# Kernel optimization log

Hardware: AMD Instinct MI355X
Metric: run time of the kernel (lower is better)

The kernel has to match this reference:

```python
import jax, jax.numpy as jnp
import numpy as np


def setup_inputs() -> dict:
    key = jax.random.key(0)
    k1, k2 = jax.random.split(key)
    N, L, C = 64, 256, 384
    x = jax.random.normal(k1, (N, L, C), dtype=jnp.float32)
    # frame counts per phoneme, 1..16
    durations = jax.random.randint(k2, (N, L), 1, 17, dtype=jnp.int32)
    # expand_max_len = max over batch of total duration (static Python int)
    mel_max_length = int(jnp.max(jnp.sum(durations, axis=-1)))
    return {"x": x, "durations": durations, "mel_max_length": mel_max_length}


def reference(x, durations, mel_max_length):
    # Equivalent to: alignment[n, t, j] = 1 if starts[n,j] <= t < csum[n,j];
    # output = alignment @ x. Implemented as a direct gather via cumulative
    # durations (searchsorted), avoiding the O(N*T*L) one-hot matmul.
    N, L, C = x.shape
    csum = jnp.cumsum(durations, axis=-1)            # [N, L] exclusive end per phoneme
    t = jnp.arange(mel_max_length)                   # [T]
    # source phoneme index for each output frame: first j with t < csum[j]
    idx = jax.vmap(lambda c: jnp.searchsorted(c, t, side='right'))(csum)  # [N, T]
    total = csum[:, -1]                              # [N] total frames per example
    valid = t[None, :] < total[:, None]              # [N, T]
    idx = jnp.minimum(idx, L - 1)
    out = jnp.take_along_axis(x, idx[..., None], axis=1)   # [N, T, C]
    out = jnp.where(valid[..., None], out, jnp.zeros((), dtype=x.dtype))
    mel_pos = jnp.arange(1, mel_max_length + 1, dtype=jnp.int64)[None, :]  # [1, T]
    return out, mel_pos
```

## Files before the change

### kernel.cpp

```cpp
#include <hip/hip_runtime.h>

#define N_B    64
#define L_IN   256
#define C_DIM  384
#define C4     (C_DIM / 4)
#define F4_PER_BLOCK 2048
#define ITERS  (F4_PER_BLOCK / 256)
#define SPLIT  4

typedef float vfloat4 __attribute__((ext_vector_type(4)));

__global__ __launch_bounds__(256) void lr_idx_kernel(const int* __restrict__ dur,
                                                     int* __restrict__ idx_out,
                                                     float* __restrict__ melpos,
                                                     int melmax) {
    __shared__ int csum[L_IN];
    const int n    = blockIdx.x & 63;
    const int part = blockIdx.x >> 6;
    const int tid  = (int)threadIdx.x;

    csum[tid] = dur[n * L_IN + tid];
    __syncthreads();
    #pragma unroll
    for (int off = 1; off < L_IN; off <<= 1) {
        int add = (tid >= off) ? csum[tid - off] : 0;
        __syncthreads();
        csum[tid] += add;
        __syncthreads();
    }
    const int total = csum[L_IN - 1];

    const int per  = (melmax + SPLIT - 1) / SPLIT;
    const int tbeg = part * per;
    const int tend = min(tbeg + per, melmax);
    for (int t = tbeg + tid; t < tend; t += 256) {
        int r = -1;
        if (t < total) {
            int lo = 0, hi = L_IN;
            #pragma unroll
            for (int s = 0; s < 8; ++s) {
                int mid = (lo + hi) >> 1;
                if (csum[mid] <= t) lo = mid + 1; else hi = mid;
            }
            r = (lo < (L_IN - 1)) ? lo : (L_IN - 1);
        }
        idx_out[n * melmax + t] = r;
        if (n == 0) melpos[t] = (float)(t + 1);
    }
}

__global__ __launch_bounds__(256) void lr_gather_kernel(const vfloat4* __restrict__ x,
                                                        const int* __restrict__ idx,
                                                        vfloat4* __restrict__ out,
                                                        int melmax, int chunks_per_n) {
    __shared__ int r_tab[32];

    const int j      = (int)blockIdx.x;
    const int xcd    = j & 7;
    const int s      = j >> 3;
    const int n      = xcd + 8 * (s / chunks_per_n);
    const int bchunk = s % chunks_per_n;
    const int tid    = (int)threadIdx.x;

    const int row_f4 = melmax * C4;
    const int start  = bchunk * F4_PER_BLOCK;
    if (start >= row_f4) return;
    const bool full  = (start + F4_PER_BLOCK) <= row_f4;
    const int end    = full ? (start + F4_PER_BLOCK) : row_f4;

    const int t0   = start / C4;
    const int tcnt = (end - 1) / C4 - t0 + 1;
    if (tid < tcnt) r_tab[tid] = idx[n * melmax + t0 + tid];
    __syncthreads();

    const size_t obase = (size_t)n * row_f4;
    if (full) {
        vfloat4 v[ITERS];
        #pragma unroll
        for (int i = 0; i < ITERS; ++i) {
            const int off = start + tid + 256 * i;
            const int t   = off / C4;
            const int c4  = off - t * C4;
            const int r   = r_tab[t - t0];
            const int rc  = (r >= 0) ? r : 0;
            vfloat4 tmp = x[(n * L_IN + rc) * C4 + c4];
            v[i] = (r >= 0) ? tmp : (vfloat4)0.f;
        }
        #pragma unroll
        for (int i = 0; i < ITERS; ++i) {
            out[obase + start + tid + 256 * i] = v[i];
        }
    } else {
        for (int off = start + tid; off < end; off += 256) {
            const int t  = off / C4;
            const int c4 = off - t * C4;
            const int r  = r_tab[t - t0];
            vfloat4 v = (vfloat4)0.f;
            if (r >= 0) v = x[(n * L_IN + r) * C4 + c4];
            out[obase + off] = v;
        }
    }
}

extern "C" void kernel_launch(void* const* d_in, const int* in_sizes, int n_in,
                              void* d_out, int out_size, void* d_ws, size_t ws_size,
                              hipStream_t stream) {
    const float* x  = (const float*)d_in[0];
    const int* dur  = (const int*)d_in[1];
    const int melmax = out_size / (N_B * C_DIM + 1);

    int* idxbuf = (int*)d_ws;
    float* mp   = (float*)d_out + (size_t)N_B * melmax * C_DIM;

    lr_idx_kernel<<<N_B * SPLIT, 256, 0, stream>>>(dur, idxbuf, mp, melmax);

    const int row_f4 = melmax * C4;
    const int chunks_per_n = (row_f4 + F4_PER_BLOCK - 1) / F4_PER_BLOCK;
    lr_gather_kernel<<<chunks_per_n * N_B, 256, 0, stream>>>(
        (const vfloat4*)x, idxbuf, (vfloat4*)d_out, melmax, chunks_per_n);
}
```

Baseline: 252.3 us.

## Fuse duration scan and index search into the gather kernel

```diff
diff --git a/kernel.cpp b/kernel.cpp
--- a/kernel.cpp
+++ b/kernel.cpp
@@ -6,53 +6,15 @@
 #define C4     (C_DIM / 4)
 #define F4_PER_BLOCK 2048
 #define ITERS  (F4_PER_BLOCK / 256)
-#define SPLIT  4
 
 typedef float vfloat4 __attribute__((ext_vector_type(4)));
 
-__global__ __launch_bounds__(256) void lr_idx_kernel(const int* __restrict__ dur,
-                                                     int* __restrict__ idx_out,
-                                                     float* __restrict__ melpos,
-                                                     int melmax) {
-    __shared__ int csum[L_IN];
-    const int n    = blockIdx.x & 63;
-    const int part = blockIdx.x >> 6;
-    const int tid  = (int)threadIdx.x;
-
-    csum[tid] = dur[n * L_IN + tid];
-    __syncthreads();
-    #pragma unroll
-    for (int off = 1; off < L_IN; off <<= 1) {
-        int add = (tid >= off) ? csum[tid - off] : 0;
-        __syncthreads();
-        csum[tid] += add;
-        __syncthreads();
-    }
-    const int total = csum[L_IN - 1];
-
-    const int per  = (melmax + SPLIT - 1) / SPLIT;
-    const int tbeg = part * per;
-    const int tend = min(tbeg + per, melmax);
-    for (int t = tbeg + tid; t < tend; t += 256) {
-        int r = -1;
-        if (t < total) {
-            int lo = 0, hi = L_IN;
-            #pragma unroll
-            for (int s = 0; s < 8; ++s) {
-                int mid = (lo + hi) >> 1;
-                if (csum[mid] <= t) lo = mid + 1; else hi = mid;
-            }
-            r = (lo < (L_IN - 1)) ? lo : (L_IN - 1);
-        }
-        idx_out[n * melmax + t] = r;
-        if (n == 0) melpos[t] = (float)(t + 1);
-    }
-}
-
-__global__ __launch_bounds__(256) void lr_gather_kernel(const vfloat4* __restrict__ x,
-                                                        const int* __restrict__ idx,
-                                                        vfloat4* __restrict__ out,
-                                                        int melmax, int chunks_per_n) {
+__global__ __launch_bounds__(256) void lr_fused_kernel(const vfloat4* __restrict__ x,
+                                                       const int* __restrict__ dur,
+                                                       vfloat4* __restrict__ out,
+                                                       float* __restrict__ melpos,
+                                                       int melmax, int chunks_per_n) {
+    __shared__ int sbuf[2][L_IN];
     __shared__ int r_tab[32];
 
     const int j      = (int)blockIdx.x;
@@ -68,9 +30,36 @@
     const bool full  = (start + F4_PER_BLOCK) <= row_f4;
     const int end    = full ? (start + F4_PER_BLOCK) : row_f4;
 
+    sbuf[0][tid] = dur[n * L_IN + tid];
+    __syncthreads();
+    int p = 0;
+    #pragma unroll
+    for (int off = 1; off < L_IN; off <<= 1) {
+        int vsum = sbuf[p][tid] + ((tid >= off) ? sbuf[p][tid - off] : 0);
+        sbuf[p ^ 1][tid] = vsum;
+        p ^= 1;
+        __syncthreads();
+    }
+    const int* csum = sbuf[p];
+    const int total = csum[L_IN - 1];
+
     const int t0   = start / C4;
     const int tcnt = (end - 1) / C4 - t0 + 1;
-    if (tid < tcnt) r_tab[tid] = idx[n * melmax + t0 + tid];
+    if (tid < tcnt) {
+        const int t = t0 + tid;
+        int r = -1;
+        if (t < total) {
+            int lo = 0, hi = L_IN;
+            #pragma unroll
+            for (int q = 0; q < 8; ++q) {
+                int mid = (lo + hi) >> 1;
+                if (csum[mid] <= t) lo = mid + 1; else hi = mid;
+            }
+            r = (lo < (L_IN - 1)) ? lo : (L_IN - 1);
+        }
+        r_tab[tid] = r;
+        if (n == 0) melpos[t] = (float)(t + 1);
+    }
     __syncthreads();
 
     const size_t obase = (size_t)n * row_f4;
@@ -109,13 +98,10 @@
     const int* dur  = (const int*)d_in[1];
     const int melmax = out_size / (N_B * C_DIM + 1);
 
-    int* idxbuf = (int*)d_ws;
-    float* mp   = (float*)d_out + (size_t)N_B * melmax * C_DIM;
-
-    lr_idx_kernel<<<N_B * SPLIT, 256, 0, stream>>>(dur, idxbuf, mp, melmax);
+    float* mp = (float*)d_out + (size_t)N_B * melmax * C_DIM;
 
     const int row_f4 = melmax * C4;
     const int chunks_per_n = (row_f4 + F4_PER_BLOCK - 1) / F4_PER_BLOCK;
-    lr_gather_kernel<<<chunks_per_n * N_B, 256, 0, stream>>>(
-        (const vfloat4*)x, idxbuf, (vfloat4*)d_out, melmax, chunks_per_n);
+    lr_fused_kernel<<<chunks_per_n * N_B, 256, 0, stream>>>(
+        (const vfloat4*)x, dur, (vfloat4*)d_out, mp, melmax, chunks_per_n);
 }
```

Measured after the change: 251.6 us, median of 2. About the same (-0.3%).
